# Kernel optimization log

Measured on AMD Instinct MI355X. Metric: run time of the kernel, lower is better.

## Reference

```python
import jax, jax.numpy as jnp
import numpy as np

KS = (3, 3)   # kernel_size
ST = (1, 1)   # stride
PD = (1, 1)   # padding
EPS = 1e-5


def unfold(x):
    """im2col matching torch.nn.Unfold: [B,C,H,W] -> [B, C*kh*kw, L] with (c,kh,kw) channel order, L row-major."""
    kh, kw = KS; sh, sw = ST; ph, pw = PD
    x = jnp.pad(x, ((0, 0), (0, 0), (ph, ph), (pw, pw)))
    B, C, H, W = x.shape
    Ho = (H - kh) // sh + 1
    Wo = (W - kw) // sw + 1
    I = (jnp.arange(Ho) * sh)[:, None, None, None] + jnp.arange(kh)[None, :, None, None]
    J = (jnp.arange(Wo) * sw)[None, None, :, None] + jnp.arange(kw)[None, None, None, :]
    p = x[:, :, I, J]  # [B, C, Ho, kh, Wo, kw]
    return p.transpose(0, 1, 3, 5, 2, 4).reshape(B, C * kh * kw, Ho * Wo)


def fold(cols, x_shape):
    """torch.nn.Fold is exactly the adjoint of Unfold (overlap-add)."""
    _, vjp = jax.vjp(unfold, jnp.zeros(x_shape, cols.dtype))
    return vjp(cols)[0]


def setup_inputs() -> dict:
    key = jax.random.key(0)
    k = jax.random.split(key, 6)
    B, C, H, W = 16, 64, 64, 64
    Cout, K = 64, KS[0] * KS[1]
    return {
        "x_mag": jax.random.uniform(k[0], (B, C, H, W), jnp.float32),
        "x_ang": jax.random.normal(k[1], (B, C, H, W), jnp.float32),
        "w_mag": jax.random.uniform(k[2], (C, K), jnp.float32),
        "w_ang": jax.random.uniform(k[3], (C, K), jnp.float32),
        "w1": jax.random.uniform(k[4], (C, K), jnp.float32),
        "w2": jax.random.uniform(k[5], (Cout, C), jnp.float32),
    }


def reference(x_mag, x_ang, w_mag, w_ang, w1, w2):
    B, C, H, W = x_mag.shape
    K = KS[0] * KS[1]
    Cout = w2.shape[0]
    Ho = (H + 2 * PD[0] - KS[0]) // ST[0] + 1
    Wo = (W + 2 * PD[1] - KS[1]) // ST[1] + 1

    # outer layer: unfold, mix with normalized weights, fold back (overlap-add)
    nws_mag = w_mag ** 2 / jnp.sum(w_mag ** 2)   # _normalize_weights_squared
    nw_ang = w_ang / jnp.sum(w_ang ** 2)         # _normalize_weights
    cm = unfold(x_mag).reshape(B, C, K, -1) + nws_mag[None, :, :, None]
    ca = unfold(x_ang).reshape(B, C, K, -1) * nw_ang[None, :, :, None]
    fm = fold(cm.reshape(B, C * K, -1), (B, C, H, W))
    fa = fold(ca.reshape(B, C * K, -1), (B, C, H, W))

    # helper: second unfold + weighted Frechet-mean reduction
    tbm = unfold(fm).reshape(B, C, K, -1)  # [B,C,K,L]
    tba = unfold(fa).reshape(B, C, K, -1)
    wmm1 = w1 ** 2 / jnp.sum(w1 ** 2, axis=1, keepdims=True)  # row-normalized
    wmm2 = w2 ** 2 / jnp.sum(w2 ** 2, axis=1, keepdims=True)
    wma1 = w1 ** 2 / jnp.sum(w1 ** 2)                          # globally normalized
    wma2 = w2 ** 2 / jnp.sum(w2 ** 2)

    m1 = jnp.einsum('bckl,ck->bcl', jnp.log(tbm + EPS), wmm1)
    out_mag = jnp.exp(jnp.einsum('bcl,oc->bol', m1, wmm2)).reshape(B, Cout, Ho, Wo)
    a1 = jnp.einsum('bckl,ck->bcl', tba, wma1)
    out_ang = jnp.einsum('bcl,oc->bol', a1, wma2).reshape(B, Cout, Ho, Wo)

    # from_polar -> stack (real, imag) on axis 1
    return jnp.stack([out_mag * jnp.cos(out_ang), out_mag * jnp.sin(out_ang)], axis=1)
```

## Files before the change

### kernel.cpp

```cpp
#include <hip/hip_runtime.h>
#include <math.h>

#define NB 16
#define NC 64
#define NL 4096
#define NCOUT 64
#define EPSF 1e-5f
#define LOG_EPSF -11.512925464970229f

#define OFF_M1 0
#define OFF_A1 (NB*NC*NL)

#define PW 72
#define PH 66

__global__ __launch_bounds__(256) void stageA_kernel(
    const float* __restrict__ x_mag, const float* __restrict__ x_ang,
    const float* __restrict__ wm, const float* __restrict__ wa,
    const float* __restrict__ w1,
    float* __restrict__ m1, float* __restrict__ a1)
{
    __shared__ float lfm[PH][PW];
    __shared__ float fas[PH][PW];
    __shared__ float smag_s[9], tang_s[9];
    __shared__ float red[3][4];

    const int tid = threadIdx.x;
    const int lane = tid & 63;
    const int wv = tid >> 6;
    const int b = blockIdx.x >> 6;
    const int c = blockIdx.x & 63;
    const int base = (b * NC + c) * NL;

    float4 xm[4], xa[4];
    #pragma unroll
    for (int k = 0; k < 4; ++k) {
        xm[k] = ((const float4*)(x_mag + base))[tid + k * 256];
        xa[k] = ((const float4*)(x_ang + base))[tid + k * 256];
    }

    float p0 = 0.f, p1 = 0.f, p2 = 0.f;
    {
        float v;
        v = wm[tid];       p0 += v * v;
        v = wm[tid + 256]; p0 += v * v;
        v = wa[tid];       p1 += v * v;
        v = wa[tid + 256]; p1 += v * v;
        v = w1[tid];       p2 += v * v;
        v = w1[tid + 256]; p2 += v * v;
        if (tid < 64) {
            v = wm[tid + 512]; p0 += v * v;
            v = wa[tid + 512]; p1 += v * v;
            v = w1[tid + 512]; p2 += v * v;
        }
    }
    #pragma unroll
    for (int s = 32; s; s >>= 1) {
        p0 += __shfl_down(p0, s);
        p1 += __shfl_down(p1, s);
        p2 += __shfl_down(p2, s);
    }
    if (lane == 0) { red[0][wv] = p0; red[1][wv] = p1; red[2][wv] = p2; }
    __syncthreads();
    const float s_wm2 = red[0][0] + red[0][1] + red[0][2] + red[0][3];
    const float s_wa2 = red[1][0] + red[1][1] + red[1][2] + red[1][3];
    const float s_w12 = red[2][0] + red[2][1] + red[2][2] + red[2][3];

    float wm1r[9], wa1r[9];
    float r1c = 0.f;
    #pragma unroll
    for (int k = 0; k < 9; ++k) { float v = w1[c * 9 + k]; wm1r[k] = v * v; r1c += v * v; }
    {
        float inv_r = 1.f / r1c, inv_s = 1.f / s_w12;
        #pragma unroll
        for (int k = 0; k < 9; ++k) { wa1r[k] = wm1r[k] * inv_s; wm1r[k] *= inv_r; }
    }

    if (tid < 9) {
        const int ci = tid / 3, cj = tid % 3;
        float sm = 0.f, sa = 0.f;
        #pragma unroll
        for (int ki = 0; ki < 3; ++ki) {
            bool vi = (ci == 0) ? (ki < 2) : ((ci == 2) ? (ki > 0) : true);
            if (!vi) continue;
            #pragma unroll
            for (int kj = 0; kj < 3; ++kj) {
                bool vj = (cj == 0) ? (kj < 2) : ((cj == 2) ? (kj > 0) : true);
                if (!vj) continue;
                float vm_ = wm[c * 9 + ki * 3 + kj];
                sm += vm_ * vm_;
                sa += wa[c * 9 + ki * 3 + kj];
            }
        }
        smag_s[tid] = sm / s_wm2;
        tang_s[tid] = sa / s_wa2;
    }

    {
        float4 sm4; sm4.x = sm4.y = sm4.z = sm4.w = LOG_EPSF;
        float4 z4;  z4.x = z4.y = z4.z = z4.w = 0.f;
        if (tid < 36) {
            int row = (tid >= 18) ? 65 : 0;
            int col4 = (tid % 18) * 4;
            *(float4*)&lfm[row][col4] = sm4;
            *(float4*)&fas[row][col4] = z4;
        } else if (tid < 164) {
            int s = tid - 36;
            int row = 1 + (s >> 1);
            int col4 = (s & 1) ? 68 : 0;
            *(float4*)&lfm[row][col4] = sm4;
            *(float4*)&fas[row][col4] = z4;
        }
    }
    __syncthreads();

    #pragma unroll
    for (int k = 0; k < 4; ++k) {
        int g = tid + k * 256;
        int i = g >> 4, j = (g & 15) * 4;
        int ci = (i == 0) ? 0 : ((i == 63) ? 2 : 1);
        float n_i = (ci == 1) ? 3.f : 2.f;
        float smC = smag_s[ci * 3 + 1], taC = tang_s[ci * 3 + 1];
        float sm[4] = { smC, smC, smC, smC };
        float ta[4] = { taC, taC, taC, taC };
        float nn[4] = { 3.f * n_i, 3.f * n_i, 3.f * n_i, 3.f * n_i };
        if (j == 0)  { sm[0] = smag_s[ci * 3 + 0]; ta[0] = tang_s[ci * 3 + 0]; nn[0] = 2.f * n_i; }
        if (j == 60) { sm[3] = smag_s[ci * 3 + 2]; ta[3] = tang_s[ci * 3 + 2]; nn[3] = 2.f * n_i; }
        float4 lo, ao;
        lo.x = __logf(fmaf(nn[0], xm[k].x, sm[0]) + EPSF);
        lo.y = __logf(fmaf(nn[1], xm[k].y, sm[1]) + EPSF);
        lo.z = __logf(fmaf(nn[2], xm[k].z, sm[2]) + EPSF);
        lo.w = __logf(fmaf(nn[3], xm[k].w, sm[3]) + EPSF);
        ao.x = xa[k].x * ta[0]; ao.y = xa[k].y * ta[1];
        ao.z = xa[k].z * ta[2]; ao.w = xa[k].w * ta[3];
        *(float4*)&lfm[i + 1][j + 4] = lo;
        *(float4*)&fas[i + 1][j + 4] = ao;
    }
    __syncthreads();

    const int i0 = (tid >> 4) * 4;
    const int j0 = (tid & 15) * 4;

    float4 accm[4], acca[4];
    #pragma unroll
    for (int li = 0; li < 4; ++li) {
        accm[li].x = accm[li].y = accm[li].z = accm[li].w = 0.f;
        acca[li].x = acca[li].y = acca[li].z = acca[li].w = 0.f;
    }

    #pragma unroll
    for (int r = 0; r < 6; ++r) {
        const int row = i0 + r;
        float4 Lm = *(const float4*)&lfm[row][j0];
        float4 Cm = *(const float4*)&lfm[row][j0 + 4];
        float4 Rm = *(const float4*)&lfm[row][j0 + 8];
        float4 La = *(const float4*)&fas[row][j0];
        float4 Ca = *(const float4*)&fas[row][j0 + 4];
        float4 Ra = *(const float4*)&fas[row][j0 + 8];
        float slm[4] = { Lm.w, Cm.x, Cm.y, Cm.z };
        float srm[4] = { Cm.y, Cm.z, Cm.w, Rm.x };
        float scm[4] = { Cm.x, Cm.y, Cm.z, Cm.w };
        float sla[4] = { La.w, Ca.x, Ca.y, Ca.z };
        float sra[4] = { Ca.y, Ca.z, Ca.w, Ra.x };
        float sca[4] = { Ca.x, Ca.y, Ca.z, Ca.w };
        #pragma unroll
        for (int ki = 0; ki < 3; ++ki) {
            const int li = r - ki;
            if (li < 0 || li > 3) continue;
            float wA = wm1r[ki * 3 + 0], wB = wm1r[ki * 3 + 1], wC = wm1r[ki * 3 + 2];
            float vA = wa1r[ki * 3 + 0], vB = wa1r[ki * 3 + 1], vC = wa1r[ki * 3 + 2];
            accm[li].x = fmaf(wA, slm[0], fmaf(wB, scm[0], fmaf(wC, srm[0], accm[li].x)));
            accm[li].y = fmaf(wA, slm[1], fmaf(wB, scm[1], fmaf(wC, srm[1], accm[li].y)));
            accm[li].z = fmaf(wA, slm[2], fmaf(wB, scm[2], fmaf(wC, srm[2], accm[li].z)));
            accm[li].w = fmaf(wA, slm[3], fmaf(wB, scm[3], fmaf(wC, srm[3], accm[li].w)));
            acca[li].x = fmaf(vA, sla[0], fmaf(vB, sca[0], fmaf(vC, sra[0], acca[li].x)));
            acca[li].y = fmaf(vA, sla[1], fmaf(vB, sca[1], fmaf(vC, sra[1], acca[li].y)));
            acca[li].z = fmaf(vA, sla[2], fmaf(vB, sca[2], fmaf(vC, sra[2], acca[li].z)));
            acca[li].w = fmaf(vA, sla[3], fmaf(vB, sca[3], fmaf(vC, sra[3], acca[li].w)));
        }
    }

    #pragma unroll
    for (int li = 0; li < 4; ++li) {
        *(float4*)&m1[base + (i0 + li) * 64 + j0] = accm[li];
        *(float4*)&a1[base + (i0 + li) * 64 + j0] = acca[li];
    }
}

#define W2P 68

#define FMA_STEP(MV, AV, WM, WA)                                                      \
    accm[0].x = fmaf(MV.x, WM.x, accm[0].x); accm[0].y = fmaf(MV.y, WM.x, accm[0].y); \
    accm[0].z = fmaf(MV.z, WM.x, accm[0].z); accm[0].w = fmaf(MV.w, WM.x, accm[0].w); \
    accm[1].x = fmaf(MV.x, WM.y, accm[1].x); accm[1].y = fmaf(MV.y, WM.y, accm[1].y); \
    accm[1].z = fmaf(MV.z, WM.y, accm[1].z); accm[1].w = fmaf(MV.w, WM.y, accm[1].w); \
    accm[2].x = fmaf(MV.x, WM.z, accm[2].x); accm[2].y = fmaf(MV.y, WM.z, accm[2].y); \
    accm[2].z = fmaf(MV.z, WM.z, accm[2].z); accm[2].w = fmaf(MV.w, WM.z, accm[2].w); \
    accm[3].x = fmaf(MV.x, WM.w, accm[3].x); accm[3].y = fmaf(MV.y, WM.w, accm[3].y); \
    accm[3].z = fmaf(MV.z, WM.w, accm[3].z); accm[3].w = fmaf(MV.w, WM.w, accm[3].w); \
    acca[0].x = fmaf(AV.x, WA.x, acca[0].x); acca[0].y = fmaf(AV.y, WA.x, acca[0].y); \
    acca[0].z = fmaf(AV.z, WA.x, acca[0].z); acca[0].w = fmaf(AV.w, WA.x, acca[0].w); \
    acca[1].x = fmaf(AV.x, WA.y, acca[1].x); acca[1].y = fmaf(AV.y, WA.y, acca[1].y); \
    acca[1].z = fmaf(AV.z, WA.y, acca[1].z); acca[1].w = fmaf(AV.w, WA.y, acca[1].w); \
    acca[2].x = fmaf(AV.x, WA.z, acca[2].x); acca[2].y = fmaf(AV.y, WA.z, acca[2].y); \
    acca[2].z = fmaf(AV.z, WA.z, acca[2].z); acca[2].w = fmaf(AV.w, WA.z, acca[2].w); \
    acca[3].x = fmaf(AV.x, WA.w, acca[3].x); acca[3].y = fmaf(AV.y, WA.w, acca[3].y); \
    acca[3].z = fmaf(AV.z, WA.w, acca[3].z); acca[3].w = fmaf(AV.w, WA.w, acca[3].w);

__global__ __launch_bounds__(256) void stageB_kernel(
    const float* __restrict__ m1, const float* __restrict__ a1,
    const float* __restrict__ w2, float* __restrict__ out)
{
    __shared__ float w2m[64][W2P];
    __shared__ float w2a[64][W2P];
    __shared__ float redB[4];

    const int tid = threadIdx.x;
    const int lane = tid & 63;
    const int wv = tid >> 6;
    const int b = blockIdx.x >> 6;
    const int lt = (blockIdx.x & 63) * 64;

    float4 v[4];
    float rpart[4];
    float s22p = 0.f;
    #pragma unroll
    for (int k = 0; k < 4; ++k) {
        int q = tid + k * 256;
        v[k] = ((const float4*)w2)[q];
        float d = fmaf(v[k].x, v[k].x, fmaf(v[k].y, v[k].y, fmaf(v[k].z, v[k].z, v[k].w * v[k].w)));
        rpart[k] = d;
        s22p += d;
    }
    #pragma unroll
    for (int k = 0; k < 4; ++k) {
        float r = rpart[k];
        r += __shfl_xor(r, 1);
        r += __shfl_xor(r, 2);
        r += __shfl_xor(r, 4);
        r += __shfl_xor(r, 8);
        rpart[k] = r;
    }
    float s = s22p;
    #pragma unroll
    for (int d = 32; d; d >>= 1) s += __shfl_down(s, d);
    if (lane == 0) redB[wv] = s;
    __syncthreads();
    const float inv_s22 = 1.f / (redB[0] + redB[1] + redB[2] + redB[3]);

    #pragma unroll
    for (int k = 0; k < 4; ++k) {
        int q = tid + k * 256;
        int o = q >> 4, c4 = (q & 15) * 4;
        float inv_r = 1.f / rpart[k];
        float sx = v[k].x * v[k].x, sy = v[k].y * v[k].y;
        float sz = v[k].z * v[k].z, sw = v[k].w * v[k].w;
        w2m[c4 + 0][o] = sx * inv_r;  w2a[c4 + 0][o] = sx * inv_s22;
        w2m[c4 + 1][o] = sy * inv_r;  w2a[c4 + 1][o] = sy * inv_s22;
        w2m[c4 + 2][o] = sz * inv_r;  w2a[c4 + 2][o] = sz * inv_s22;
        w2m[c4 + 3][o] = sw * inv_r;  w2a[c4 + 3][o] = sw * inv_s22;
    }
    __syncthreads();

    const int l0 = (tid & 15) * 4;
    const int o0 = (tid >> 4) * 4;

    float4 accm[4], acca[4];
    #pragma unroll
    for (int oi = 0; oi < 4; ++oi) {
        accm[oi].x = accm[oi].y = accm[oi].z = accm[oi].w = 0.f;
        acca[oi].x = acca[oi].y = acca[oi].z = acca[oi].w = 0.f;
    }

    const float* m1p = m1 + (size_t)b * NC * NL + lt + l0;
    const float* a1p = a1 + (size_t)b * NC * NL + lt + l0;

    float4 mvA = *(const float4*)(m1p);
    float4 avA = *(const float4*)(a1p);
    float4 mvB = *(const float4*)(m1p + NL);
    float4 avB = *(const float4*)(a1p + NL);

    #pragma unroll 2
    for (int c = 0; c < 62; ++c) {
        float4 mvN = *(const float4*)(m1p + (c + 2) * NL);
        float4 avN = *(const float4*)(a1p + (c + 2) * NL);
        float4 wm_ = *(const float4*)&w2m[c][o0];
        float4 wa_ = *(const float4*)&w2a[c][o0];
        FMA_STEP(mvA, avA, wm_, wa_);
        mvA = mvB; avA = avB;
        mvB = mvN; avB = avN;
    }
    {
        float4 wm_ = *(const float4*)&w2m[62][o0];
        float4 wa_ = *(const float4*)&w2a[62][o0];
        FMA_STEP(mvA, avA, wm_, wa_);
    }
    {
        float4 wm_ = *(const float4*)&w2m[63][o0];
        float4 wa_ = *(const float4*)&w2a[63][o0];
        FMA_STEP(mvB, avB, wm_, wa_);
    }

    #pragma unroll
    for (int oi = 0; oi < 4; ++oi) {
        const int o = o0 + oi;
        float4 mg, oc, os;
        mg.x = __expf(accm[oi].x); mg.y = __expf(accm[oi].y);
        mg.z = __expf(accm[oi].z); mg.w = __expf(accm[oi].w);
        oc.x = mg.x * __cosf(acca[oi].x); os.x = mg.x * __sinf(acca[oi].x);
        oc.y = mg.y * __cosf(acca[oi].y); os.y = mg.y * __sinf(acca[oi].y);
        oc.z = mg.z * __cosf(acca[oi].z); os.z = mg.z * __sinf(acca[oi].z);
        oc.w = mg.w * __cosf(acca[oi].w); os.w = mg.w * __sinf(acca[oi].w);
        size_t gi = ((size_t)(b * 2) * NCOUT + o) * NL + lt + l0;
        *(float4*)&out[gi] = oc;
        *(float4*)&out[gi + (size_t)NCOUT * NL] = os;
    }
}

extern "C" void kernel_launch(void* const* d_in, const int* in_sizes, int n_in,
                              void* d_out, int out_size, void* d_ws, size_t ws_size,
                              hipStream_t stream) {
    const float* x_mag = (const float*)d_in[0];
    const float* x_ang = (const float*)d_in[1];
    const float* w_mag = (const float*)d_in[2];
    const float* w_ang = (const float*)d_in[3];
    const float* w1    = (const float*)d_in[4];
    const float* w2    = (const float*)d_in[5];
    float* out = (float*)d_out;
    float* ws  = (float*)d_ws;

    float* m1 = ws + OFF_M1;
    float* a1 = ws + OFF_A1;

    stageA_kernel<<<NB * NC, 256, 0, stream>>>(x_mag, x_ang, w_mag, w_ang, w1, m1, a1);
    stageB_kernel<<<NB * 64, 256, 0, stream>>>(m1, a1, w2, out);
}
```

Measured before the change: 45.25 us.

## Fuse stencil stage and channel-mix stage into one row-tiled kernel

Merges the two kernels into one: each block handles one output row of one batch, streams input channels in chunks of four through shared memory, computes the 3x3 stencil into small shared buffers, and immediately accumulates the 64x64 channel mix. This removes the m1/a1 intermediate round trip through global memory and one launch. In exchange, each block re-reads three input rows per channel (halo overhead), recomputes weight normalisation per block, and adds two barriers per chunk. Block index is also swizzled.

```diff
diff --git a/kernel.cpp b/kernel.cpp
--- a/kernel.cpp
+++ b/kernel.cpp
@@ -7,187 +7,8 @@
 #define NCOUT 64
 #define EPSF 1e-5f
 #define LOG_EPSF -11.512925464970229f
-
-#define OFF_M1 0
-#define OFF_A1 (NB*NC*NL)
-
-#define PW 72
-#define PH 66
-
-__global__ __launch_bounds__(256) void stageA_kernel(
-    const float* __restrict__ x_mag, const float* __restrict__ x_ang,
-    const float* __restrict__ wm, const float* __restrict__ wa,
-    const float* __restrict__ w1,
-    float* __restrict__ m1, float* __restrict__ a1)
-{
-    __shared__ float lfm[PH][PW];
-    __shared__ float fas[PH][PW];
-    __shared__ float smag_s[9], tang_s[9];
-    __shared__ float red[3][4];
-
-    const int tid = threadIdx.x;
-    const int lane = tid & 63;
-    const int wv = tid >> 6;
-    const int b = blockIdx.x >> 6;
-    const int c = blockIdx.x & 63;
-    const int base = (b * NC + c) * NL;
-
-    float4 xm[4], xa[4];
-    #pragma unroll
-    for (int k = 0; k < 4; ++k) {
-        xm[k] = ((const float4*)(x_mag + base))[tid + k * 256];
-        xa[k] = ((const float4*)(x_ang + base))[tid + k * 256];
-    }
-
-    float p0 = 0.f, p1 = 0.f, p2 = 0.f;
-    {
-        float v;
-        v = wm[tid];       p0 += v * v;
-        v = wm[tid + 256]; p0 += v * v;
-        v = wa[tid];       p1 += v * v;
-        v = wa[tid + 256]; p1 += v * v;
-        v = w1[tid];       p2 += v * v;
-        v = w1[tid + 256]; p2 += v * v;
-        if (tid < 64) {
-            v = wm[tid + 512]; p0 += v * v;
-            v = wa[tid + 512]; p1 += v * v;
-            v = w1[tid + 512]; p2 += v * v;
-        }
-    }
-    #pragma unroll
-    for (int s = 32; s; s >>= 1) {
-        p0 += __shfl_down(p0, s);
-        p1 += __shfl_down(p1, s);
-        p2 += __shfl_down(p2, s);
-    }
-    if (lane == 0) { red[0][wv] = p0; red[1][wv] = p1; red[2][wv] = p2; }
-    __syncthreads();
-    const float s_wm2 = red[0][0] + red[0][1] + red[0][2] + red[0][3];
-    const float s_wa2 = red[1][0] + red[1][1] + red[1][2] + red[1][3];
-    const float s_w12 = red[2][0] + red[2][1] + red[2][2] + red[2][3];
-
-    float wm1r[9], wa1r[9];
-    float r1c = 0.f;
-    #pragma unroll
-    for (int k = 0; k < 9; ++k) { float v = w1[c * 9 + k]; wm1r[k] = v * v; r1c += v * v; }
-    {
-        float inv_r = 1.f / r1c, inv_s = 1.f / s_w12;
-        #pragma unroll
-        for (int k = 0; k < 9; ++k) { wa1r[k] = wm1r[k] * inv_s; wm1r[k] *= inv_r; }
-    }
-
-    if (tid < 9) {
-        const int ci = tid / 3, cj = tid % 3;
-        float sm = 0.f, sa = 0.f;
-        #pragma unroll
-        for (int ki = 0; ki < 3; ++ki) {
-            bool vi = (ci == 0) ? (ki < 2) : ((ci == 2) ? (ki > 0) : true);
-            if (!vi) continue;
-            #pragma unroll
-            for (int kj = 0; kj < 3; ++kj) {
-                bool vj = (cj == 0) ? (kj < 2) : ((cj == 2) ? (kj > 0) : true);
-                if (!vj) continue;
-                float vm_ = wm[c * 9 + ki * 3 + kj];
-                sm += vm_ * vm_;
-                sa += wa[c * 9 + ki * 3 + kj];
-            }
-        }
-        smag_s[tid] = sm / s_wm2;
-        tang_s[tid] = sa / s_wa2;
-    }
-
-    {
-        float4 sm4; sm4.x = sm4.y = sm4.z = sm4.w = LOG_EPSF;
-        float4 z4;  z4.x = z4.y = z4.z = z4.w = 0.f;
-        if (tid < 36) {
-            int row = (tid >= 18) ? 65 : 0;
-            int col4 = (tid % 18) * 4;
-            *(float4*)&lfm[row][col4] = sm4;
-            *(float4*)&fas[row][col4] = z4;
-        } else if (tid < 164) {
-            int s = tid - 36;
-            int row = 1 + (s >> 1);
-            int col4 = (s & 1) ? 68 : 0;
-            *(float4*)&lfm[row][col4] = sm4;
-            *(float4*)&fas[row][col4] = z4;
-        }
-    }
-    __syncthreads();
-
-    #pragma unroll
-    for (int k = 0; k < 4; ++k) {
-        int g = tid + k * 256;
-        int i = g >> 4, j = (g & 15) * 4;
-        int ci = (i == 0) ? 0 : ((i == 63) ? 2 : 1);
-        float n_i = (ci == 1) ? 3.f : 2.f;
-        float smC = smag_s[ci * 3 + 1], taC = tang_s[ci * 3 + 1];
-        float sm[4] = { smC, smC, smC, smC };
-        float ta[4] = { taC, taC, taC, taC };
-        float nn[4] = { 3.f * n_i, 3.f * n_i, 3.f * n_i, 3.f * n_i };
-        if (j == 0)  { sm[0] = smag_s[ci * 3 + 0]; ta[0] = tang_s[ci * 3 + 0]; nn[0] = 2.f * n_i; }
-        if (j == 60) { sm[3] = smag_s[ci * 3 + 2]; ta[3] = tang_s[ci * 3 + 2]; nn[3] = 2.f * n_i; }
-        float4 lo, ao;
-        lo.x = __logf(fmaf(nn[0], xm[k].x, sm[0]) + EPSF);
-        lo.y = __logf(fmaf(nn[1], xm[k].y, sm[1]) + EPSF);
-        lo.z = __logf(fmaf(nn[2], xm[k].z, sm[2]) + EPSF);
-        lo.w = __logf(fmaf(nn[3], xm[k].w, sm[3]) + EPSF);
-        ao.x = xa[k].x * ta[0]; ao.y = xa[k].y * ta[1];
-        ao.z = xa[k].z * ta[2]; ao.w = xa[k].w * ta[3];
-        *(float4*)&lfm[i + 1][j + 4] = lo;
-        *(float4*)&fas[i + 1][j + 4] = ao;
-    }
-    __syncthreads();
-
-    const int i0 = (tid >> 4) * 4;
-    const int j0 = (tid & 15) * 4;
-
-    float4 accm[4], acca[4];
-    #pragma unroll
-    for (int li = 0; li < 4; ++li) {
-        accm[li].x = accm[li].y = accm[li].z = accm[li].w = 0.f;
-        acca[li].x = acca[li].y = acca[li].z = acca[li].w = 0.f;
-    }
-
-    #pragma unroll
-    for (int r = 0; r < 6; ++r) {
-        const int row = i0 + r;
-        float4 Lm = *(const float4*)&lfm[row][j0];
-        float4 Cm = *(const float4*)&lfm[row][j0 + 4];
-        float4 Rm = *(const float4*)&lfm[row][j0 + 8];
-        float4 La = *(const float4*)&fas[row][j0];
-        float4 Ca = *(const float4*)&fas[row][j0 + 4];
-        float4 Ra = *(const float4*)&fas[row][j0 + 8];
-        float slm[4] = { Lm.w, Cm.x, Cm.y, Cm.z };
-        float srm[4] = { Cm.y, Cm.z, Cm.w, Rm.x };
-        float scm[4] = { Cm.x, Cm.y, Cm.z, Cm.w };
-        float sla[4] = { La.w, Ca.x, Ca.y, Ca.z };
-        float sra[4] = { Ca.y, Ca.z, Ca.w, Ra.x };
-        float sca[4] = { Ca.x, Ca.y, Ca.z, Ca.w };
-        #pragma unroll
-        for (int ki = 0; ki < 3; ++ki) {
-            const int li = r - ki;
-            if (li < 0 || li > 3) continue;
-            float wA = wm1r[ki * 3 + 0], wB = wm1r[ki * 3 + 1], wC = wm1r[ki * 3 + 2];
-            float vA = wa1r[ki * 3 + 0], vB = wa1r[ki * 3 + 1], vC = wa1r[ki * 3 + 2];
-            accm[li].x = fmaf(wA, slm[0], fmaf(wB, scm[0], fmaf(wC, srm[0], accm[li].x)));
-            accm[li].y = fmaf(wA, slm[1], fmaf(wB, scm[1], fmaf(wC, srm[1], accm[li].y)));
-            accm[li].z = fmaf(wA, slm[2], fmaf(wB, scm[2], fmaf(wC, srm[2], accm[li].z)));
-            accm[li].w = fmaf(wA, slm[3], fmaf(wB, scm[3], fmaf(wC, srm[3], accm[li].w)));
-            acca[li].x = fmaf(vA, sla[0], fmaf(vB, sca[0], fmaf(vC, sra[0], acca[li].x)));
-            acca[li].y = fmaf(vA, sla[1], fmaf(vB, sca[1], fmaf(vC, sra[1], acca[li].y)));
-            acca[li].z = fmaf(vA, sla[2], fmaf(vB, sca[2], fmaf(vC, sra[2], acca[li].z)));
-            acca[li].w = fmaf(vA, sla[3], fmaf(vB, sca[3], fmaf(vC, sra[3], acca[li].w)));
-        }
-    }
-
-    #pragma unroll
-    for (int li = 0; li < 4; ++li) {
-        *(float4*)&m1[base + (i0 + li) * 64 + j0] = accm[li];
-        *(float4*)&a1[base + (i0 + li) * 64 + j0] = acca[li];
-    }
-}
-
-#define W2P 68
+#define CC 4
+#define NCHUNK 16
 
 #define FMA_STEP(MV, AV, WM, WA)                                                      \
     accm[0].x = fmaf(MV.x, WM.x, accm[0].x); accm[0].y = fmaf(MV.y, WM.x, accm[0].y); \
@@ -207,63 +28,162 @@
     acca[3].x = fmaf(AV.x, WA.w, acca[3].x); acca[3].y = fmaf(AV.y, WA.w, acca[3].y); \
     acca[3].z = fmaf(AV.z, WA.w, acca[3].z); acca[3].w = fmaf(AV.w, WA.w, acca[3].w);
 
-__global__ __launch_bounds__(256) void stageB_kernel(
-    const float* __restrict__ m1, const float* __restrict__ a1,
-    const float* __restrict__ w2, float* __restrict__ out)
+__global__ __launch_bounds__(256, 3) void fused_kernel(
+    const float* __restrict__ x_mag, const float* __restrict__ x_ang,
+    const float* __restrict__ wm, const float* __restrict__ wa,
+    const float* __restrict__ w1, const float* __restrict__ w2,
+    float* __restrict__ out)
 {
-    __shared__ float w2m[64][W2P];
-    __shared__ float w2a[64][W2P];
-    __shared__ float redB[4];
+    __shared__ float lfm[CC][3][72];
+    __shared__ float fas[CC][3][72];
+    __shared__ float m1r[CC][64];
+    __shared__ float a1r[CC][64];
+    __shared__ float w2m[64][68];
+    __shared__ float w2a[64][68];
+    __shared__ float wm1s[64][9];
+    __shared__ float wa1s[64][9];
+    __shared__ float smag_s[64][9];
+    __shared__ float tang_s[64][9];
+    __shared__ float red[4][4];
 
     const int tid = threadIdx.x;
     const int lane = tid & 63;
     const int wv = tid >> 6;
-    const int b = blockIdx.x >> 6;
-    const int lt = (blockIdx.x & 63) * 64;
-
-    float4 v[4];
-    float rpart[4];
-    float s22p = 0.f;
+
+    int bid = (blockIdx.x & 7) * 128 + (blockIdx.x >> 3);
+    const int b = bid >> 6;
+    const int i = bid & 63;
+
+    const bool mag0 = (tid < 192);
+    const int m0 = mag0 ? tid : tid - 192;
+    const int cl0 = m0 / 48;
+    const int rm0 = m0 - cl0 * 48;
+    const int r0 = rm0 >> 4, j40 = rm0 & 15;
+    const int ir0 = i - 1 + r0;
+    const bool ok0 = ((unsigned)ir0 < 64u);
+    const float* sp0 = (mag0 ? x_mag : x_ang)
+                     + ((size_t)(b * NC + cl0) * NL + (ok0 ? ir0 : 0) * 64 + j40 * 4);
+
+    const bool has1 = (tid < 128);
+    const int it1 = tid + 64;
+    const int cl1 = it1 / 48;
+    const int rm1 = it1 - cl1 * 48;
+    const int r1 = rm1 >> 4, j41 = rm1 & 15;
+    const int ir1 = i - 1 + r1;
+    const bool ok1 = has1 && ((unsigned)ir1 < 64u);
+    const float* sp1 = x_ang + ((size_t)(b * NC + cl1) * NL + (ok1 ? ir1 : 0) * 64 + j41 * 4);
+
+    float4 pf0 = *(const float4*)sp0;
+    float4 pf1;
+    if (has1) pf1 = *(const float4*)sp1;
+
+    const int ci0 = (ir0 == 0) ? 0 : ((ir0 == 63) ? 2 : 1);
+    const float ni0 = (ci0 == 1) ? 3.f : 2.f;
+    const int kL0 = ci0 * 3 + 0, kC0 = ci0 * 3 + 1, kR0 = ci0 * 3 + 2;
+    const float nC0 = 3.f * ni0;
+    const float n00 = (j40 == 0) ? 2.f * ni0 : nC0;
+    const float n30 = (j40 == 15) ? 2.f * ni0 : nC0;
+    const int ci1 = (ir1 == 0) ? 0 : ((ir1 == 63) ? 2 : 1);
+    const int kL1 = ci1 * 3 + 0, kC1 = ci1 * 3 + 1, kR1 = ci1 * 3 + 2;
+
+    float p0 = 0.f, p1 = 0.f, p2 = 0.f, p3 = 0.f;
+    {
+        float v;
+        v = wm[tid];       p0 += v * v;  v = wm[tid + 256]; p0 += v * v;
+        v = wa[tid];       p1 += v * v;  v = wa[tid + 256]; p1 += v * v;
+        v = w1[tid];       p2 += v * v;  v = w1[tid + 256]; p2 += v * v;
+        if (tid < 64) {
+            v = wm[tid + 512]; p0 += v * v;
+            v = wa[tid + 512]; p1 += v * v;
+            v = w1[tid + 512]; p2 += v * v;
+        }
+    }
+    float4 v4[4]; float rpart[4];
     #pragma unroll
     for (int k = 0; k < 4; ++k) {
         int q = tid + k * 256;
-        v[k] = ((const float4*)w2)[q];
-        float d = fmaf(v[k].x, v[k].x, fmaf(v[k].y, v[k].y, fmaf(v[k].z, v[k].z, v[k].w * v[k].w)));
-        rpart[k] = d;
-        s22p += d;
+        v4[k] = ((const float4*)w2)[q];
+        float d = fmaf(v4[k].x, v4[k].x, fmaf(v4[k].y, v4[k].y,
+                  fmaf(v4[k].z, v4[k].z, v4[k].w * v4[k].w)));
+        rpart[k] = d; p3 += d;
     }
     #pragma unroll
     for (int k = 0; k < 4; ++k) {
         float r = rpart[k];
-        r += __shfl_xor(r, 1);
-        r += __shfl_xor(r, 2);
-        r += __shfl_xor(r, 4);
-        r += __shfl_xor(r, 8);
+        r += __shfl_xor(r, 1); r += __shfl_xor(r, 2);
+        r += __shfl_xor(r, 4); r += __shfl_xor(r, 8);
         rpart[k] = r;
     }
-    float s = s22p;
-    #pragma unroll
-    for (int d = 32; d; d >>= 1) s += __shfl_down(s, d);
-    if (lane == 0) redB[wv] = s;
+    #pragma unroll
+    for (int s = 32; s; s >>= 1) {
+        p0 += __shfl_down(p0, s); p1 += __shfl_down(p1, s);
+        p2 += __shfl_down(p2, s); p3 += __shfl_down(p3, s);
+    }
+    if (lane == 0) { red[0][wv] = p0; red[1][wv] = p1; red[2][wv] = p2; red[3][wv] = p3; }
     __syncthreads();
-    const float inv_s22 = 1.f / (redB[0] + redB[1] + redB[2] + redB[3]);
+    const float s_wm2 = red[0][0] + red[0][1] + red[0][2] + red[0][3];
+    const float s_wa2 = red[1][0] + red[1][1] + red[1][2] + red[1][3];
+    const float s_w12 = red[2][0] + red[2][1] + red[2][2] + red[2][3];
+    const float inv_s22 = 1.f / (red[3][0] + red[3][1] + red[3][2] + red[3][3]);
 
     #pragma unroll
     for (int k = 0; k < 4; ++k) {
         int q = tid + k * 256;
         int o = q >> 4, c4 = (q & 15) * 4;
         float inv_r = 1.f / rpart[k];
-        float sx = v[k].x * v[k].x, sy = v[k].y * v[k].y;
-        float sz = v[k].z * v[k].z, sw = v[k].w * v[k].w;
+        float sx = v4[k].x * v4[k].x, sy = v4[k].y * v4[k].y;
+        float sz = v4[k].z * v4[k].z, sw = v4[k].w * v4[k].w;
         w2m[c4 + 0][o] = sx * inv_r;  w2a[c4 + 0][o] = sx * inv_s22;
         w2m[c4 + 1][o] = sy * inv_r;  w2a[c4 + 1][o] = sy * inv_s22;
         w2m[c4 + 2][o] = sz * inv_r;  w2a[c4 + 2][o] = sz * inv_s22;
         w2m[c4 + 3][o] = sw * inv_r;  w2a[c4 + 3][o] = sw * inv_s22;
     }
+    if (tid < 64) {
+        const int c = tid;
+        float q[9]; float r1c = 0.f;
+        #pragma unroll
+        for (int k = 0; k < 9; ++k) { float v = w1[c * 9 + k]; q[k] = v * v; r1c += q[k]; }
+        float inv_r = 1.f / r1c, inv_s = 1.f / s_w12;
+        #pragma unroll
+        for (int k = 0; k < 9; ++k) { wm1s[c][k] = q[k] * inv_r; wa1s[c][k] = q[k] * inv_s; }
+    } else if (tid < 128) {
+        const int c = tid - 64;
+        float nm[9], na[9];
+        float inv_m = 1.f / s_wm2, inv_a = 1.f / s_wa2;
+        #pragma unroll
+        for (int k = 0; k < 9; ++k) {
+            float v = wm[c * 9 + k];
+            nm[k] = v * v * inv_m;
+            na[k] = wa[c * 9 + k] * inv_a;
+        }
+        #pragma unroll
+        for (int ci = 0; ci < 3; ++ci) {
+            #pragma unroll
+            for (int cj = 0; cj < 3; ++cj) {
+                float sm = 0.f, sa = 0.f;
+                #pragma unroll
+                for (int ki = 0; ki < 3; ++ki) {
+                    bool vi = (ci == 0) ? (ki < 2) : ((ci == 2) ? (ki > 0) : true);
+                    if (!vi) continue;
+                    #pragma unroll
+                    for (int kj = 0; kj < 3; ++kj) {
+                        bool vj = (cj == 0) ? (kj < 2) : ((cj == 2) ? (kj > 0) : true);
+                        if (!vj) continue;
+                        sm += nm[ki * 3 + kj];
+                        sa += na[ki * 3 + kj];
+                    }
+                }
+                smag_s[c][ci * 3 + cj] = sm;
+                tang_s[c][ci * 3 + cj] = sa;
+            }
+        }
+    }
     __syncthreads();
 
     const int l0 = (tid & 15) * 4;
     const int o0 = (tid >> 4) * 4;
+    const int cv_c = tid >> 6;
+    const int cv_j = tid & 63;
 
     float4 accm[4], acca[4];
     #pragma unroll
@@ -272,33 +192,91 @@
         acca[oi].x = acca[oi].y = acca[oi].z = acca[oi].w = 0.f;
     }
 
-    const float* m1p = m1 + (size_t)b * NC * NL + lt + l0;
-    const float* a1p = a1 + (size_t)b * NC * NL + lt + l0;
-
-    float4 mvA = *(const float4*)(m1p);
-    float4 avA = *(const float4*)(a1p);
-    float4 mvB = *(const float4*)(m1p + NL);
-    float4 avB = *(const float4*)(a1p + NL);
-
-    #pragma unroll 2
-    for (int c = 0; c < 62; ++c) {
-        float4 mvN = *(const float4*)(m1p + (c + 2) * NL);
-        float4 avN = *(const float4*)(a1p + (c + 2) * NL);
-        float4 wm_ = *(const float4*)&w2m[c][o0];
-        float4 wa_ = *(const float4*)&w2a[c][o0];
-        FMA_STEP(mvA, avA, wm_, wa_);
-        mvA = mvB; avA = avB;
-        mvB = mvN; avB = avN;
-    }
-    {
-        float4 wm_ = *(const float4*)&w2m[62][o0];
-        float4 wa_ = *(const float4*)&w2a[62][o0];
-        FMA_STEP(mvA, avA, wm_, wa_);
-    }
-    {
-        float4 wm_ = *(const float4*)&w2m[63][o0];
-        float4 wa_ = *(const float4*)&w2a[63][o0];
-        FMA_STEP(mvB, avB, wm_, wa_);
+    for (int ch = 0; ch < NCHUNK; ++ch) {
+        const int ch0 = ch * CC;
+
+        {
+            const int c0g = ch0 + cl0;
+            if (mag0) {
+                float4 dv;
+                if (ok0) {
+                    float sC = smag_s[c0g][kC0];
+                    float s0 = (j40 == 0)  ? smag_s[c0g][kL0] : sC;
+                    float s3 = (j40 == 15) ? smag_s[c0g][kR0] : sC;
+                    dv.x = __logf(fmaf(n00, pf0.x, s0) + EPSF);
+                    dv.y = __logf(fmaf(nC0, pf0.y, sC) + EPSF);
+                    dv.z = __logf(fmaf(nC0, pf0.z, sC) + EPSF);
+                    dv.w = __logf(fmaf(n30, pf0.w, s3) + EPSF);
+                } else {
+                    dv.x = dv.y = dv.z = dv.w = LOG_EPSF;
+                }
+                *(float4*)&lfm[cl0][r0][4 + j40 * 4] = dv;
+                if (j40 == 0)  lfm[cl0][r0][3]  = LOG_EPSF;
+                if (j40 == 15) lfm[cl0][r0][68] = LOG_EPSF;
+            } else {
+                float4 dv;
+                if (ok0) {
+                    float tC = tang_s[c0g][kC0];
+                    float t0 = (j40 == 0)  ? tang_s[c0g][kL0] : tC;
+                    float t3 = (j40 == 15) ? tang_s[c0g][kR0] : tC;
+                    dv.x = pf0.x * t0; dv.y = pf0.y * tC;
+                    dv.z = pf0.z * tC; dv.w = pf0.w * t3;
+                } else {
+                    dv.x = dv.y = dv.z = dv.w = 0.f;
+                }
+                *(float4*)&fas[cl0][r0][4 + j40 * 4] = dv;
+                if (j40 == 0)  fas[cl0][r0][3]  = 0.f;
+                if (j40 == 15) fas[cl0][r0][68] = 0.f;
+            }
+            if (has1) {
+                const int c1g = ch0 + cl1;
+                float4 dv;
+                if (ok1) {
+                    float tC = tang_s[c1g][kC1];
+                    float t0 = (j41 == 0)  ? tang_s[c1g][kL1] : tC;
+                    float t3 = (j41 == 15) ? tang_s[c1g][kR1] : tC;
+                    dv.x = pf1.x * t0; dv.y = pf1.y * tC;
+                    dv.z = pf1.z * tC; dv.w = pf1.w * t3;
+                } else {
+                    dv.x = dv.y = dv.z = dv.w = 0.f;
+                }
+                *(float4*)&fas[cl1][r1][4 + j41 * 4] = dv;
+                if (j41 == 0)  fas[cl1][r1][3]  = 0.f;
+                if (j41 == 15) fas[cl1][r1][68] = 0.f;
+            }
+        }
+
+        if (ch + 1 < NCHUNK) {
+            const size_t adv = (size_t)(ch + 1) * CC * NL;
+            pf0 = *(const float4*)(sp0 + adv);
+            if (has1) pf1 = *(const float4*)(sp1 + adv);
+        }
+        __syncthreads();
+
+        {
+            const int cg = ch0 + cv_c;
+            float am = 0.f, aa = 0.f;
+            #pragma unroll
+            for (int r = 0; r < 3; ++r) {
+                #pragma unroll
+                for (int dj = 0; dj < 3; ++dj) {
+                    am = fmaf(wm1s[cg][r * 3 + dj], lfm[cv_c][r][cv_j + 3 + dj], am);
+                    aa = fmaf(wa1s[cg][r * 3 + dj], fas[cv_c][r][cv_j + 3 + dj], aa);
+                }
+            }
+            m1r[cv_c][cv_j] = am;
+            a1r[cv_c][cv_j] = aa;
+        }
+        __syncthreads();
+
+        #pragma unroll
+        for (int cc = 0; cc < CC; ++cc) {
+            float4 mv = *(const float4*)&m1r[cc][l0];
+            float4 av = *(const float4*)&a1r[cc][l0];
+            float4 wmv = *(const float4*)&w2m[ch0 + cc][o0];
+            float4 wav = *(const float4*)&w2a[ch0 + cc][o0];
+            FMA_STEP(mv, av, wmv, wav);
+        }
     }
 
     #pragma unroll
@@ -311,7 +289,7 @@
         oc.y = mg.y * __cosf(acca[oi].y); os.y = mg.y * __sinf(acca[oi].y);
         oc.z = mg.z * __cosf(acca[oi].z); os.z = mg.z * __sinf(acca[oi].z);
         oc.w = mg.w * __cosf(acca[oi].w); os.w = mg.w * __sinf(acca[oi].w);
-        size_t gi = ((size_t)(b * 2) * NCOUT + o) * NL + lt + l0;
+        size_t gi = ((size_t)(b * 2) * NCOUT + o) * NL + i * 64 + l0;
         *(float4*)&out[gi] = oc;
         *(float4*)&out[gi + (size_t)NCOUT * NL] = os;
     }
@@ -327,11 +305,6 @@
     const float* w1    = (const float*)d_in[4];
     const float* w2    = (const float*)d_in[5];
     float* out = (float*)d_out;
-    float* ws  = (float*)d_ws;
-
-    float* m1 = ws + OFF_M1;
-    float* a1 = ws + OFF_A1;
-
-    stageA_kernel<<<NB * NC, 256, 0, stream>>>(x_mag, x_ang, w_mag, w_ang, w1, m1, a1);
-    stageB_kernel<<<NB * 64, 256, 0, stream>>>(m1, a1, w2, out);
+
+    fused_kernel<<<NB * 64, 256, 0, stream>>>(x_mag, x_ang, w_mag, w_ang, w1, w2, out);
 }
```

Measured after the change: 50.89 us. +12.5%, slower.
